# Kernel tuning notes

Measured on AMD Instinct MI355X. Metric: run time of the kernel, lower is better.

The kernel has to match this reference:

```python
import jax, jax.numpy as jnp
import numpy as np

N = 3072      # number of EDU nodes in the document
H = 256       # opt.tree_hid_him
NREL = 18     # relation classes (hardcoded in rel_clf)
ALPHA = 0.25


def setup_inputs() -> dict:
    key = jax.random.key(0)
    ks = jax.random.split(key, 20)
    s = 0.02
    all_edus = jax.random.normal(ks[0], (1, N, H), jnp.float32)
    # dependency tree: child i (1..N-1) has parent < i
    children_ids = jnp.arange(1, N, dtype=jnp.int32)
    parents_ids = (jax.random.randint(ks[1], (N - 1,), 0, N) % jnp.maximum(children_ids, 1)).astype(jnp.int32)
    half = (N - 1) // 2
    left_adj = jnp.zeros((N, N), jnp.float32).at[parents_ids[:half], children_ids[:half]].set(1.0)
    right_adj = jnp.zeros((N, N), jnp.float32).at[parents_ids[half:], children_ids[half:]].set(1.0)
    rels = jax.random.randint(ks[2], (N - 1,), 1, NREL).astype(jnp.int32)  # all nonzero -> rels[rels!=0] == rels
    return dict(
        all_edus=all_edus,
        left_adj=left_adj,
        right_adj=right_adj,
        W_bilin=jax.random.normal(ks[3], (2, H, H), jnp.float32) * s,
        b_bilin=jnp.zeros((2,), jnp.float32),
        W_head=jax.random.normal(ks[4], (2, H), jnp.float32) * s,
        W_dep=jax.random.normal(ks[5], (2, H), jnp.float32) * s,
        Wr1=jax.random.normal(ks[6], (H, H), jnp.float32) * s,
        br1=jnp.zeros((H,), jnp.float32),
        Wr2=jax.random.normal(ks[7], (H, 1), jnp.float32) * s,
        br2=jnp.zeros((1,), jnp.float32),
        Wrel1=jax.random.normal(ks[8], (2 * H, H), jnp.float32) * s,
        brel1=jnp.zeros((H,), jnp.float32),
        Wrel2=jax.random.normal(ks[9], (H, NREL), jnp.float32) * s,
        brel2=jnp.zeros((NREL,), jnp.float32),
        children_ids=children_ids,
        parents_ids=parents_ids,
        rels=rels,
        true_root=0,
    )


def reference(all_edus, left_adj, right_adj, W_bilin, b_bilin, W_head, W_dep,
              Wr1, br1, Wr2, br2, Wrel1, brel1, Wrel2, brel2,
              children_ids, parents_ids, rels, true_root):
    x = all_edus[0]                                      # [N, H]
    # --- get_compat_matrix: compat[i, j, k] = bilin_k(h_i, h_j) + head_k(h_i) + dep_k(h_j) ---
    compat = (jnp.einsum('ih,khd,jd->ijk', x, W_bilin, x) + b_bilin
              + (x @ W_head.T)[:, None, :] + (x @ W_dep.T)[None, :, :])  # [N, N, 2]
    # --- root_clf ---
    g = jax.nn.gelu(x @ Wr1 + br1, approximate=False)
    root_scores = g @ Wr2 + br2                          # [N, 1]
    # --- logistic_loss (matrix-tree theorem) ---
    gold = (root_scores[true_root, 0]
            + jnp.sum(compat[:, :, 0] * left_adj)
            + jnp.sum(compat[:, :, 1] * right_adj))
    A = jnp.exp(compat).sum(axis=-1)                     # [N, N]
    lap = jnp.diag(A.sum(axis=0)) - A                    # diag of column sums (torch sum over dim=1)
    lap = lap.at[0, :].set(jnp.exp(root_scores[:, 0]))
    sign, logabs = jnp.linalg.slogdet(lap)
    logdet = jnp.where(sign > 0, logabs, jnp.nan)        # torch.logdet semantics
    notnan = ((~jnp.isnan(gold)) & (~jnp.isnan(logdet))).astype(lap.dtype)
    mask = (gold <= logdet * notnan).astype(lap.dtype)
    loss = (logdet - gold) * mask
    loss = jnp.where(jnp.isnan(loss), 0.0, loss)
    log_loss = ALPHA * loss
    # --- rels_loss: edge-indexed gather + MLP + CE(sum) ---
    feats = jnp.concatenate([x[parents_ids], x[children_ids]], axis=1)  # [E, 2H]
    h = jax.nn.gelu(feats @ Wrel1 + brel1, approximate=False)
    logits = h @ Wrel2 + brel2                           # [E, 18]
    logp = jax.nn.log_softmax(logits, axis=-1)
    ce = -jnp.sum(jnp.take_along_axis(logp, rels[:, None].astype(jnp.int32), axis=1))
    return log_loss + ce
```

## Files before the change

### kernel.cpp

```cpp
#include <hip/hip_runtime.h>
#include <math.h>

#define N 3072
#define H 256
#define NRELS 18
#define EDGES (N-1)
#define HALF ((N-1)/2)
#define NB 64
#define NSTEP (N/NB)

static const size_t OFF_M   = 0;
static const size_t OFF_Y   = (size_t)N*N;
static const size_t OFF_XH  = OFF_Y + (size_t)4*N*H;
static const size_t OFF_XD  = OFF_XH + (size_t)2*N;
static const size_t OFF_RS  = OFF_XD + (size_t)2*N;
static const size_t OFF_CS  = OFF_RS + (size_t)N;
static const size_t OFF_ACC = OFF_CS + (size_t)N;
static const size_t OFF_IAC = OFF_ACC + 8;

__device__ __forceinline__ float gelu_exact(float a){
    return 0.5f*a*(1.0f + erff(a*0.70710678118654752440f));
}

__global__ void k_init(float* cs, float* acc, int* iacc){
    int t = blockIdx.x*256 + threadIdx.x;
    if(t < N) cs[t] = 0.f;
    if(t < 8) acc[t] = 0.f;
    if(t < 4) iacc[t] = 0;
}

__global__ __launch_bounds__(256) void k_xhd(const float* __restrict__ x,
        const float* __restrict__ Wh, const float* __restrict__ Wd,
        float* __restrict__ xh, float* __restrict__ xd){
    __shared__ float xs[H];
    int i = blockIdx.x, t = threadIdx.x;
    xs[t] = x[(size_t)i*H + t];
    __syncthreads();
    int w = t >> 6, lane = t & 63;
    const float* Wrow = (w==0)? Wh : (w==1)? Wh+H : (w==2)? Wd : Wd+H;
    float s = 0.f;
    #pragma unroll
    for(int q=0;q<4;q++) s += xs[lane+64*q]*Wrow[lane+64*q];
    #pragma unroll
    for(int off=32;off>0;off>>=1) s += __shfl_down(s, off, 64);
    if(lane==0){ if(w<2) xh[i*2+w]=s; else xd[i*2+(w-2)]=s; }
}

__global__ __launch_bounds__(256) void k_root(const float* __restrict__ x,
        const float* __restrict__ Wr1, const float* __restrict__ br1,
        const float* __restrict__ Wr2, const float* __restrict__ br2,
        float* __restrict__ rs){
    __shared__ float xs[H];
    __shared__ float red[256];
    int i = blockIdx.x, t = threadIdx.x;
    xs[t] = x[(size_t)i*H + t];
    __syncthreads();
    float a = br1[t];
    for(int d=0; d<H; d++) a += xs[d]*Wr1[(size_t)d*H + t];
    red[t] = gelu_exact(a)*Wr2[t];
    __syncthreads();
    for(int s=128;s>0;s>>=1){ if(t<s) red[t]+=red[t+s]; __syncthreads(); }
    if(t==0) rs[i] = red[0] + br2[0];
}

__global__ __launch_bounds__(256) void k_mats(const float* __restrict__ x,
        const float* __restrict__ Wb, const float* __restrict__ Wrel1,
        float* __restrict__ Yout){
    __shared__ float xs[H];
    int i = blockIdx.x, m = blockIdx.y, t = threadIdx.x;
    xs[t] = x[(size_t)i*H + t];
    __syncthreads();
    const float* W = (m==0)? Wb : (m==1)? Wb + (size_t)H*H
                   : (m==2)? Wrel1 : Wrel1 + (size_t)H*H;
    float acc = 0.f;
    for(int h=0; h<H; h++) acc += xs[h]*W[(size_t)h*H + t];
    Yout[(size_t)m*N*H + (size_t)i*H + t] = acc;
}

__global__ __launch_bounds__(256) void k_compatA(
        const float* __restrict__ x, const float* __restrict__ Y0,
        const float* __restrict__ Y1, const float* __restrict__ xh,
        const float* __restrict__ xd, const float* __restrict__ bb,
        float* __restrict__ M){
    __shared__ float a0s[16][65], a1s[16][65], bs[16][65];
    int i0 = blockIdx.y*64, j0 = blockIdx.x*64;
    int t = threadIdx.x;
    int tx = t & 15, ty = t >> 4;
    float c0[4][4] = {}, c1[4][4] = {};
    for(int k0=0; k0<H; k0+=16){
        int kk = t & 15, r0 = t >> 4;
        for(int rr=r0; rr<64; rr+=16){
            a0s[kk][rr] = Y0[(size_t)(i0+rr)*H + k0+kk];
            a1s[kk][rr] = Y1[(size_t)(i0+rr)*H + k0+kk];
            bs [kk][rr] = x [(size_t)(j0+rr)*H + k0+kk];
        }
        __syncthreads();
        #pragma unroll
        for(int kk2=0; kk2<16; kk2++){
            float ar0[4], ar1[4], br[4];
            #pragma unroll
            for(int u=0;u<4;u++){ ar0[u]=a0s[kk2][ty*4+u]; ar1[u]=a1s[kk2][ty*4+u]; }
            #pragma unroll
            for(int v=0;v<4;v++) br[v]=bs[kk2][tx*4+v];
            #pragma unroll
            for(int u=0;u<4;u++)
                #pragma unroll
                for(int v=0;v<4;v++){ c0[u][v]+=ar0[u]*br[v]; c1[u][v]+=ar1[u]*br[v]; }
        }
        __syncthreads();
    }
    float b0 = bb[0], b1 = bb[1];
    #pragma unroll
    for(int u=0;u<4;u++){
        int i = i0 + ty*4 + u;
        float h0 = xh[2*i], h1 = xh[2*i+1];
        int pi = (i==0)? N-1 : i-1;
        #pragma unroll
        for(int v=0;v<4;v++){
            int j = j0 + tx*4 + v;
            int pj = (j==0)? N-1 : j-1;
            float cc0 = c0[u][v] + b0 + h0 + xd[2*j];
            float cc1 = c1[u][v] + b1 + h1 + xd[2*j+1];
            M[(size_t)pi*N + pj] = -(expf(cc0)+expf(cc1));
        }
    }
}

__global__ __launch_bounds__(256) void k_gold(const float* __restrict__ x,
        const float* __restrict__ Y, const float* __restrict__ xh,
        const float* __restrict__ xd, const float* __restrict__ bb,
        const int* __restrict__ par, const int* __restrict__ chi,
        float* __restrict__ acc){
    int w = threadIdx.x >> 6, lane = threadIdx.x & 63;
    int e = blockIdx.x*4 + w;
    if(e >= EDGES) return;
    int p = par[e], c = chi[e];
    int k = (e < HALF)? 0 : 1;
    const float* Yk = Y + (size_t)k*N*H;
    float s = 0.f;
    #pragma unroll
    for(int q=0;q<4;q++)
        s += Yk[(size_t)p*H + lane+64*q]*x[(size_t)c*H + lane+64*q];
    #pragma unroll
    for(int off=32;off>0;off>>=1) s += __shfl_down(s, off, 64);
    if(lane==0) atomicAdd(acc+0, s + bb[k] + xh[2*p+k] + xd[2*c+k]);
}

__global__ __launch_bounds__(256) void k_ce(
        const float* __restrict__ Pm, const float* __restrict__ Qm,
        const float* __restrict__ brel1, const float* __restrict__ Wrel2,
        const float* __restrict__ brel2, const int* __restrict__ par,
        const int* __restrict__ chi, const int* __restrict__ rels,
        float* __restrict__ acc){
    __shared__ float red[256][NRELS+1];
    int e = blockIdx.x, t = threadIdx.x;
    int p = par[e], c = chi[e];
    float a = Pm[(size_t)p*H + t] + Qm[(size_t)c*H + t] + brel1[t];
    float h = gelu_exact(a);
    #pragma unroll
    for(int r=0;r<NRELS;r++) red[t][r] = h*Wrel2[t*NRELS + r];
    __syncthreads();
    for(int s=128;s>0;s>>=1){
        if(t<s){
            #pragma unroll
            for(int r=0;r<NRELS;r++) red[t][r] += red[t+s][r];
        }
        __syncthreads();
    }
    if(t==0){
        int rsel = rels[e];
        float mx = -1e30f;
        for(int r=0;r<NRELS;r++) mx = fmaxf(mx, red[0][r]+brel2[r]);
        float se = 0.f;
        for(int r=0;r<NRELS;r++) se += expf(red[0][r]+brel2[r]-mx);
        float lse = mx + logf(se);
        atomicAdd(acc+2, lse - (red[0][rsel]+brel2[rsel]));
    }
}

__global__ __launch_bounds__(256) void k_colsum(const float* __restrict__ M,
        float* __restrict__ cs){
    int c = blockIdx.x*256 + threadIdx.x;
    int r0 = blockIdx.y*(N/16);
    float s = 0.f;
    for(int r=r0; r<r0+N/16; r++) s += M[(size_t)r*N + c];
    atomicAdd(cs+c, s);
}

__global__ __launch_bounds__(256) void k_fix(float* __restrict__ M,
        const float* __restrict__ cs, const float* __restrict__ rs){
    int c = blockIdx.x*256 + threadIdx.x;
    if(c < N-1) M[(size_t)c*N + c] -= cs[c];
    int oj = (c==N-1)? 0 : c+1;
    M[(size_t)(N-1)*N + c] = expf(rs[oj]);
}

__global__ __launch_bounds__(256) void k_lu_diag(float* __restrict__ M, int K0,
        float* __restrict__ acc, int* __restrict__ iacc){
    __shared__ float D[NB][NB+1];
    __shared__ float lcol[NB];
    int t = threadIdx.x;
    for(int e=t; e<NB*NB; e+=256){ int r=e>>6, c=e&63; D[r][c] = M[(size_t)(K0+r)*N + K0+c]; }
    __syncthreads();
    for(int j=0;j<NB;j++){
        if(t>j && t<NB){ float l = D[t][j]/D[j][j]; D[t][j]=l; lcol[t]=l; }
        __syncthreads();
        int ty = t>>4, tx = t&15;
        for(int ii=j+1+ty; ii<NB; ii+=16){
            float l = lcol[ii];
            for(int cc=j+1+tx; cc<NB; cc+=16) D[ii][cc] -= l*D[j][cc];
        }
        __syncthreads();
    }
    if(t==0){
        float s = 0.f; int neg=0, zer=0;
        for(int j=0;j<NB;j++){
            float v = D[j][j];
            s += logf(fabsf(v));
            if(v < 0.f) neg++;
            if(v == 0.f) zer++;
        }
        atomicAdd(acc+1, s);
        if(neg) atomicAdd(iacc+0, neg);
        if(zer) atomicAdd(iacc+1, zer);
    }
    __syncthreads();
    for(int e=t; e<NB*NB; e+=256){ int r=e>>6, c=e&63; M[(size_t)(K0+r)*N + K0+c] = D[r][c]; }
}

__global__ __launch_bounds__(128) void k_lu_panel(float* __restrict__ M, int K0){
    __shared__ float Dd[NB][NB+1];
    __shared__ float Tl[128][NB+1];
    int t = threadIdx.x;
    int m = N - K0 - NB;
    int nch = (m + 127)/128;
    for(int e=t; e<NB*NB; e+=128){ int r=e>>6, c=e&63; Dd[r][c] = M[(size_t)(K0+r)*N + K0+c]; }
    __syncthreads();
    if((int)blockIdx.x < nch){
        int base = K0 + NB + blockIdx.x*128;
        for(int e=t; e<128*NB; e+=128){ int rr=e>>6, cc=e&63;
            int row = base+rr; Tl[rr][cc] = (row<N)? M[(size_t)row*N + K0+cc] : 0.f; }
        __syncthreads();
        int row = base + t;
        if(row < N){
            float a[NB];
            #pragma unroll
            for(int c=0;c<NB;c++) a[c] = Tl[t][c];
            #pragma unroll
            for(int c=0;c<NB;c++){
                float xc = a[c]/Dd[c][c];
                a[c] = xc;
                #pragma unroll
                for(int cc=c+1;cc<NB;cc++) a[cc] -= xc*Dd[c][cc];
            }
            #pragma unroll
            for(int c=0;c<NB;c++) Tl[t][c] = a[c];
        }
        __syncthreads();
        for(int e=t; e<128*NB; e+=128){ int rr=e>>6, cc=e&63;
            int row2 = base+rr; if(row2<N) M[(size_t)row2*N + K0+cc] = Tl[rr][cc]; }
    } else {
        int cbase = K0 + NB + (blockIdx.x - nch)*128;
        for(int e=t; e<NB*128; e+=128){ int rr=e>>7, cc=e&127;
            int col = cbase+cc; Tl[cc][rr] = (col<N)? M[(size_t)(K0+rr)*N + col] : 0.f; }
        __syncthreads();
        int col = cbase + t;
        if(col < N){
            float a[NB];
            #pragma unroll
            for(int r=0;r<NB;r++) a[r] = Tl[t][r];
            #pragma unroll
            for(int r=0;r<NB;r++){
                float ur = a[r];
                #pragma unroll
                for(int rr=r+1;rr<NB;rr++) a[rr] -= ur*Dd[rr][r];
            }
            #pragma unroll
            for(int r=0;r<NB;r++) Tl[t][r] = a[r];
        }
        __syncthreads();
        for(int e=t; e<NB*128; e+=128){ int rr=e>>7, cc=e&127;
            int col2 = cbase+cc; if(col2<N) M[(size_t)(K0+rr)*N + col2] = Tl[cc][rr]; }
    }
}

__global__ __launch_bounds__(256) void k_lu_update(float* __restrict__ M, int K0){
    __shared__ float As[16][65], Bs[16][65];
    int base = K0 + NB;
    int ii0 = base + blockIdx.y*64;
    int jj0 = base + blockIdx.x*64;
    int t = threadIdx.x, tx = t&15, ty = t>>4;
    float c[4][4] = {};
    for(int k0=0; k0<NB; k0+=16){
        {
            int kk = t&15, r0 = t>>4;
            for(int rr=r0; rr<64; rr+=16)
                As[kk][rr] = M[(size_t)(ii0+rr)*N + K0+k0+kk];
        }
        {
            int cc = t&63, kr = t>>6;
            for(int k2=kr; k2<16; k2+=4)
                Bs[k2][cc] = M[(size_t)(K0+k0+k2)*N + jj0+cc];
        }
        __syncthreads();
        #pragma unroll
        for(int kk2=0; kk2<16; kk2++){
            float ar[4], br[4];
            #pragma unroll
            for(int u=0;u<4;u++) ar[u] = As[kk2][ty*4+u];
            #pragma unroll
            for(int v=0;v<4;v++) br[v] = Bs[kk2][tx*4+v];
            #pragma unroll
            for(int u=0;u<4;u++)
                #pragma unroll
                for(int v=0;v<4;v++) c[u][v] += ar[u]*br[v];
        }
        __syncthreads();
    }
    #pragma unroll
    for(int u=0;u<4;u++)
        #pragma unroll
        for(int v=0;v<4;v++){
            size_t idx = (size_t)(ii0+ty*4+u)*N + jj0+tx*4+v;
            M[idx] -= c[u][v];
        }
}

__global__ void k_final(const float* __restrict__ acc, const int* __restrict__ iacc,
        const float* __restrict__ rs, const int* __restrict__ troot,
        float* __restrict__ out){
    float gold = acc[0] + rs[troot[0]];
    float logabs = acc[1];
    bool pos = (iacc[1]==0) && ((iacc[0]&1)==0);
    float logdet = pos ? logabs : __builtin_nanf("");
    float notnan = (!isnan(gold) && !isnan(logdet)) ? 1.f : 0.f;
    float mv = logdet*notnan;
    float mask = (gold <= mv) ? 1.f : 0.f;
    float loss = (logdet - gold)*mask;
    if(isnan(loss)) loss = 0.f;
    out[0] = 0.25f*loss + acc[2];
}

extern "C" void kernel_launch(void* const* d_in, const int* in_sizes, int n_in,
                              void* d_out, int out_size, void* d_ws, size_t ws_size,
                              hipStream_t stream){
    const float* x     = (const float*)d_in[0];
    const float* Wb    = (const float*)d_in[3];
    const float* bb    = (const float*)d_in[4];
    const float* Wh    = (const float*)d_in[5];
    const float* Wd    = (const float*)d_in[6];
    const float* Wr1   = (const float*)d_in[7];
    const float* br1   = (const float*)d_in[8];
    const float* Wr2   = (const float*)d_in[9];
    const float* br2   = (const float*)d_in[10];
    const float* Wrel1 = (const float*)d_in[11];
    const float* brel1 = (const float*)d_in[12];
    const float* Wrel2 = (const float*)d_in[13];
    const float* brel2 = (const float*)d_in[14];
    const int* chi   = (const int*)d_in[15];
    const int* par   = (const int*)d_in[16];
    const int* rels  = (const int*)d_in[17];
    const int* troot = (const int*)d_in[18];

    float* ws = (float*)d_ws;
    float* M  = ws + OFF_M;
    float* Y  = ws + OFF_Y;
    float* Y0 = Y;
    float* Y1 = Y + (size_t)N*H;
    float* Pm = Y + (size_t)2*N*H;
    float* Qm = Y + (size_t)3*N*H;
    float* xh = ws + OFF_XH;
    float* xd = ws + OFF_XD;
    float* rs = ws + OFF_RS;
    float* cs = ws + OFF_CS;
    float* acc = ws + OFF_ACC;
    int*   iacc = (int*)(ws + OFF_IAC);
    float* out = (float*)d_out;

    k_init<<<N/256, 256, 0, stream>>>(cs, acc, iacc);
    k_xhd<<<N, 256, 0, stream>>>(x, Wh, Wd, xh, xd);
    k_root<<<N, 256, 0, stream>>>(x, Wr1, br1, Wr2, br2, rs);
    k_mats<<<dim3(N,4), 256, 0, stream>>>(x, Wb, Wrel1, Y);
    k_compatA<<<dim3(N/64, N/64), 256, 0, stream>>>(x, Y0, Y1, xh, xd, bb, M);
    k_gold<<<(EDGES+3)/4, 256, 0, stream>>>(x, Y, xh, xd, bb, par, chi, acc);
    k_ce<<<EDGES, 256, 0, stream>>>(Pm, Qm, brel1, Wrel2, brel2, par, chi, rels, acc);
    k_colsum<<<dim3(N/256, 16), 256, 0, stream>>>(M, cs);
    k_fix<<<N/256, 256, 0, stream>>>(M, cs, rs);

    k_lu_diag<<<1, 256, 0, stream>>>(M, 0, acc, iacc);
    for(int kb=0; kb<NSTEP-1; kb++){
        int K0 = kb*NB;
        int m  = N - K0 - NB;
        int nch = (m + 127)/128;
        k_lu_panel<<<2*nch, 128, 0, stream>>>(M, K0);
        dim3 g(m/64, m/64);
        k_lu_update<<<g, 256, 0, stream>>>(M, K0);
        k_lu_diag<<<1, 256, 0, stream>>>(M, K0+NB, acc, iacc);
    }
    k_final<<<1, 1, 0, stream>>>(acc, iacc, rs, troot, out);
}
```

Measured before the change: 5.500 ms.

## Fuse blocked LU loop into one persistent kernel with grid-wide barriers

Replaces the per-step diag, panel and update kernel launches of the blocked LU with a single persistent kernel. Its grid is sized from occupancy, and the steps are separated by an atomic-counter grid barrier. The next diagonal block is now factored by whichever block handles update tile 0, which removes the separate single-block diag launch. Panel work is split into 64-wide chunks where only 64 threads compute. The kernel relies on all blocks being co-resident for the spin barrier to be safe, and it adds barrier latency in place of launch gaps.

```diff
diff --git a/kernel.cpp b/kernel.cpp
--- a/kernel.cpp
+++ b/kernel.cpp
@@ -20,6 +20,24 @@
 
 __device__ __forceinline__ float gelu_exact(float a){
     return 0.5f*a*(1.0f + erff(a*0.70710678118654752440f));
+}
+
+__device__ __forceinline__ void gsync(int* bar){
+    __syncthreads();
+    if(threadIdx.x == 0){
+        __threadfence();
+        int g = __hip_atomic_load(bar+1, __ATOMIC_RELAXED, __HIP_MEMORY_SCOPE_AGENT);
+        int v = __hip_atomic_fetch_add(bar, 1, __ATOMIC_ACQ_REL, __HIP_MEMORY_SCOPE_AGENT);
+        if(v == (int)gridDim.x - 1){
+            __hip_atomic_store(bar, 0, __ATOMIC_RELAXED, __HIP_MEMORY_SCOPE_AGENT);
+            __hip_atomic_fetch_add(bar+1, 1, __ATOMIC_RELEASE, __HIP_MEMORY_SCOPE_AGENT);
+        } else {
+            while(__hip_atomic_load(bar+1, __ATOMIC_ACQUIRE, __HIP_MEMORY_SCOPE_AGENT) == g)
+                __builtin_amdgcn_s_sleep(4);
+        }
+        __threadfence();
+    }
+    __syncthreads();
 }
 
 __global__ void k_init(float* cs, float* acc, int* iacc){
@@ -195,13 +213,8 @@
     M[(size_t)(N-1)*N + c] = expf(rs[oj]);
 }
 
-__global__ __launch_bounds__(256) void k_lu_diag(float* __restrict__ M, int K0,
-        float* __restrict__ acc, int* __restrict__ iacc){
-    __shared__ float D[NB][NB+1];
-    __shared__ float lcol[NB];
-    int t = threadIdx.x;
-    for(int e=t; e<NB*NB; e+=256){ int r=e>>6, c=e&63; D[r][c] = M[(size_t)(K0+r)*N + K0+c]; }
-    __syncthreads();
+__device__ __forceinline__ void factor_diag(float (*D)[NB+1], float* lcol, int t,
+        float* acc, int* iacc){
     for(int j=0;j<NB;j++){
         if(t>j && t<NB){ float l = D[t][j]/D[j][j]; D[t][j]=l; lcol[t]=l; }
         __syncthreads();
@@ -225,105 +238,149 @@
         if(zer) atomicAdd(iacc+1, zer);
     }
     __syncthreads();
-    for(int e=t; e<NB*NB; e+=256){ int r=e>>6, c=e&63; M[(size_t)(K0+r)*N + K0+c] = D[r][c]; }
-}
-
-__global__ __launch_bounds__(128) void k_lu_panel(float* __restrict__ M, int K0){
-    __shared__ float Dd[NB][NB+1];
-    __shared__ float Tl[128][NB+1];
+}
+
+__global__ __launch_bounds__(256, 2) void k_lu(float* __restrict__ M,
+        float* __restrict__ acc, int* __restrict__ iacc, int* __restrict__ bar){
+    __shared__ float smem[8320];
     int t = threadIdx.x;
-    int m = N - K0 - NB;
-    int nch = (m + 127)/128;
-    for(int e=t; e<NB*NB; e+=128){ int r=e>>6, c=e&63; Dd[r][c] = M[(size_t)(K0+r)*N + K0+c]; }
-    __syncthreads();
-    if((int)blockIdx.x < nch){
-        int base = K0 + NB + blockIdx.x*128;
-        for(int e=t; e<128*NB; e+=128){ int rr=e>>6, cc=e&63;
-            int row = base+rr; Tl[rr][cc] = (row<N)? M[(size_t)row*N + K0+cc] : 0.f; }
-        __syncthreads();
-        int row = base + t;
-        if(row < N){
-            float a[NB];
-            #pragma unroll
-            for(int c=0;c<NB;c++) a[c] = Tl[t][c];
-            #pragma unroll
-            for(int c=0;c<NB;c++){
-                float xc = a[c]/Dd[c][c];
-                a[c] = xc;
-                #pragma unroll
-                for(int cc=c+1;cc<NB;cc++) a[cc] -= xc*Dd[c][cc];
+
+    if(blockIdx.x == 0){
+        float (*D)[NB+1] = (float(*)[NB+1])smem;
+        float* lcol = smem + 4160;
+        for(int e=t; e<NB*NB; e+=256){ int r=e>>6, c=e&63; D[r][c] = M[(size_t)r*N + c]; }
+        __syncthreads();
+        factor_diag(D, lcol, t, acc, iacc);
+        for(int e=t; e<NB*NB; e+=256){ int r=e>>6, c=e&63; M[(size_t)r*N + c] = D[r][c]; }
+    }
+    gsync(bar);
+
+    for(int kb=0; kb<NSTEP-1; kb++){
+        int K0 = kb*NB;
+        int m  = N - K0 - NB;
+        int base = K0 + NB;
+
+        {
+            float (*Dd)[NB+1] = (float(*)[NB+1])smem;
+            float (*T)[NB+1]  = (float(*)[NB+1])(smem + 4160);
+            int nch = m >> 6;
+            int tot = 2*nch;
+            for(int ch = blockIdx.x; ch < tot; ch += gridDim.x){
+                for(int e=t; e<NB*NB; e+=256){ int r=e>>6, c=e&63;
+                    Dd[r][c] = M[(size_t)(K0+r)*N + K0+c]; }
+                if(ch < nch){
+                    int rbase = base + ch*NB;
+                    for(int e=t; e<NB*NB; e+=256){ int rr=e>>6, cc=e&63;
+                        T[rr][cc] = M[(size_t)(rbase+rr)*N + K0+cc]; }
+                    __syncthreads();
+                    if(t < NB){
+                        float a[NB];
+                        #pragma unroll
+                        for(int c=0;c<NB;c++) a[c] = T[t][c];
+                        #pragma unroll
+                        for(int c=0;c<NB;c++){
+                            float xc = a[c]/Dd[c][c];
+                            a[c] = xc;
+                            #pragma unroll
+                            for(int cc=c+1;cc<NB;cc++) a[cc] -= xc*Dd[c][cc];
+                        }
+                        #pragma unroll
+                        for(int c=0;c<NB;c++) T[t][c] = a[c];
+                    }
+                    __syncthreads();
+                    for(int e=t; e<NB*NB; e+=256){ int rr=e>>6, cc=e&63;
+                        M[(size_t)(rbase+rr)*N + K0+cc] = T[rr][cc]; }
+                } else {
+                    int cbase = base + (ch-nch)*NB;
+                    for(int e=t; e<NB*NB; e+=256){ int r=e>>6, cl=e&63;
+                        T[cl][r] = M[(size_t)(K0+r)*N + cbase+cl]; }
+                    __syncthreads();
+                    if(t < NB){
+                        float a[NB];
+                        #pragma unroll
+                        for(int r=0;r<NB;r++) a[r] = T[t][r];
+                        #pragma unroll
+                        for(int r=0;r<NB;r++){
+                            float ur = a[r];
+                            #pragma unroll
+                            for(int rr=r+1;rr<NB;rr++) a[rr] -= ur*Dd[rr][r];
+                        }
+                        #pragma unroll
+                        for(int r=0;r<NB;r++) T[t][r] = a[r];
+                    }
+                    __syncthreads();
+                    for(int e=t; e<NB*NB; e+=256){ int r=e>>6, cl=e&63;
+                        M[(size_t)(K0+r)*N + cbase+cl] = T[cl][r]; }
+                }
+                __syncthreads();
             }
-            #pragma unroll
-            for(int c=0;c<NB;c++) Tl[t][c] = a[c];
-        }
-        __syncthreads();
-        for(int e=t; e<128*NB; e+=128){ int rr=e>>6, cc=e&63;
-            int row2 = base+rr; if(row2<N) M[(size_t)row2*N + K0+cc] = Tl[rr][cc]; }
-    } else {
-        int cbase = K0 + NB + (blockIdx.x - nch)*128;
-        for(int e=t; e<NB*128; e+=128){ int rr=e>>7, cc=e&127;
-            int col = cbase+cc; Tl[cc][rr] = (col<N)? M[(size_t)(K0+rr)*N + col] : 0.f; }
-        __syncthreads();
-        int col = cbase + t;
-        if(col < N){
-            float a[NB];
-            #pragma unroll
-            for(int r=0;r<NB;r++) a[r] = Tl[t][r];
-            #pragma unroll
-            for(int r=0;r<NB;r++){
-                float ur = a[r];
-                #pragma unroll
-                for(int rr=r+1;rr<NB;rr++) a[rr] -= ur*Dd[rr][r];
+        }
+        gsync(bar);
+
+        {
+            float (*As)[NB+1] = (float(*)[NB+1])smem;
+            float (*Bs)[NB+1] = (float(*)[NB+1])(smem + 1040);
+            float (*D)[NB+1]  = (float(*)[NB+1])(smem + 2080);
+            float* lcol = smem + 6240;
+            int nt = m >> 6;
+            int ntiles = nt*nt;
+            for(int tau = blockIdx.x; tau < ntiles; tau += gridDim.x){
+                int ti = tau/nt, tj = tau - ti*nt;
+                int ii0 = base + ti*64, jj0 = base + tj*64;
+                int tx = t&15, ty = t>>4;
+                float c[4][4] = {};
+                for(int k0=0; k0<NB; k0+=16){
+                    {
+                        int kk = t&15, r0 = t>>4;
+                        for(int rr=r0; rr<64; rr+=16)
+                            As[kk][rr] = M[(size_t)(ii0+rr)*N + K0+k0+kk];
+                    }
+                    {
+                        int cc = t&63, kr = t>>6;
+                        for(int k2=kr; k2<16; k2+=4)
+                            Bs[k2][cc] = M[(size_t)(K0+k0+k2)*N + jj0+cc];
+                    }
+                    __syncthreads();
+                    #pragma unroll
+                    for(int kk2=0; kk2<16; kk2++){
+                        float ar[4], br[4];
+                        #pragma unroll
+                        for(int u=0;u<4;u++) ar[u] = As[kk2][ty*4+u];
+                        #pragma unroll
+                        for(int v=0;v<4;v++) br[v] = Bs[kk2][tx*4+v];
+                        #pragma unroll
+                        for(int u=0;u<4;u++)
+                            #pragma unroll
+                            for(int v=0;v<4;v++) c[u][v] += ar[u]*br[v];
+                    }
+                    __syncthreads();
+                }
+                if(tau == 0){
+                    #pragma unroll
+                    for(int u=0;u<4;u++)
+                        #pragma unroll
+                        for(int v=0;v<4;v++){
+                            size_t idx = (size_t)(ii0+ty*4+u)*N + jj0+tx*4+v;
+                            D[ty*4+u][tx*4+v] = M[idx] - c[u][v];
+                        }
+                    __syncthreads();
+                    factor_diag(D, lcol, t, acc, iacc);
+                    for(int e=t; e<NB*NB; e+=256){ int r=e>>6, cc2=e&63;
+                        M[(size_t)(base+r)*N + base+cc2] = D[r][cc2]; }
+                } else {
+                    #pragma unroll
+                    for(int u=0;u<4;u++)
+                        #pragma unroll
+                        for(int v=0;v<4;v++){
+                            size_t idx = (size_t)(ii0+ty*4+u)*N + jj0+tx*4+v;
+                            M[idx] -= c[u][v];
+                        }
+                }
+                __syncthreads();
             }
-            #pragma unroll
-            for(int r=0;r<NB;r++) Tl[t][r] = a[r];
-        }
-        __syncthreads();
-        for(int e=t; e<NB*128; e+=128){ int rr=e>>7, cc=e&127;
-            int col2 = cbase+cc; if(col2<N) M[(size_t)(K0+rr)*N + col2] = Tl[cc][rr]; }
-    }
-}
-
-__global__ __launch_bounds__(256) void k_lu_update(float* __restrict__ M, int K0){
-    __shared__ float As[16][65], Bs[16][65];
-    int base = K0 + NB;
-    int ii0 = base + blockIdx.y*64;
-    int jj0 = base + blockIdx.x*64;
-    int t = threadIdx.x, tx = t&15, ty = t>>4;
-    float c[4][4] = {};
-    for(int k0=0; k0<NB; k0+=16){
-        {
-            int kk = t&15, r0 = t>>4;
-            for(int rr=r0; rr<64; rr+=16)
-                As[kk][rr] = M[(size_t)(ii0+rr)*N + K0+k0+kk];
-        }
-        {
-            int cc = t&63, kr = t>>6;
-            for(int k2=kr; k2<16; k2+=4)
-                Bs[k2][cc] = M[(size_t)(K0+k0+k2)*N + jj0+cc];
-        }
-        __syncthreads();
-        #pragma unroll
-        for(int kk2=0; kk2<16; kk2++){
-            float ar[4], br[4];
-            #pragma unroll
-            for(int u=0;u<4;u++) ar[u] = As[kk2][ty*4+u];
-            #pragma unroll
-            for(int v=0;v<4;v++) br[v] = Bs[kk2][tx*4+v];
-            #pragma unroll
-            for(int u=0;u<4;u++)
-                #pragma unroll
-                for(int v=0;v<4;v++) c[u][v] += ar[u]*br[v];
-        }
-        __syncthreads();
-    }
-    #pragma unroll
-    for(int u=0;u<4;u++)
-        #pragma unroll
-        for(int v=0;v<4;v++){
-            size_t idx = (size_t)(ii0+ty*4+u)*N + jj0+tx*4+v;
-            M[idx] -= c[u][v];
-        }
+        }
+        gsync(bar);
+    }
 }
 
 __global__ void k_final(const float* __restrict__ acc, const int* __restrict__ iacc,
@@ -375,6 +432,7 @@
     float* cs = ws + OFF_CS;
     float* acc = ws + OFF_ACC;
     int*   iacc = (int*)(ws + OFF_IAC);
+    int*   bar  = (int*)(acc + 4);
     float* out = (float*)d_out;
 
     k_init<<<N/256, 256, 0, stream>>>(cs, acc, iacc);
@@ -387,15 +445,19 @@
     k_colsum<<<dim3(N/256, 16), 256, 0, stream>>>(M, cs);
     k_fix<<<N/256, 256, 0, stream>>>(M, cs, rs);
 
-    k_lu_diag<<<1, 256, 0, stream>>>(M, 0, acc, iacc);
-    for(int kb=0; kb<NSTEP-1; kb++){
-        int K0 = kb*NB;
-        int m  = N - K0 - NB;
-        int nch = (m + 127)/128;
-        k_lu_panel<<<2*nch, 128, 0, stream>>>(M, K0);
-        dim3 g(m/64, m/64);
-        k_lu_update<<<g, 256, 0, stream>>>(M, K0);
-        k_lu_diag<<<1, 256, 0, stream>>>(M, K0+NB, acc, iacc);
-    }
+    static int lu_grid = 0;
+    if(lu_grid == 0){
+        int occ = 0;
+        hipOccupancyMaxActiveBlocksPerMultiprocessor(&occ, k_lu, 256, 0);
+        if(occ < 1) occ = 1;
+        int ncu = 0;
+        hipDeviceGetAttribute(&ncu, hipDeviceAttributeMultiprocessorCount, 0);
+        if(ncu <= 0) ncu = 256;
+        long g = (long)occ * ncu;
+        if(g > 512) g = 512;
+        lu_grid = (int)g;
+    }
+    k_lu<<<lu_grid, 256, 0, stream>>>(M, acc, iacc, bar);
+
     k_final<<<1, 1, 0, stream>>>(acc, iacc, rs, troot, out);
 }
```

Measured after the change: 11.43 ms. 108% more time.
